# Kernel optimization log

Hardware: AMD Instinct MI355X
Metric: run time of the kernel (lower is better)

Reference implementation:

```python
import jax, jax.numpy as jnp
import numpy as np

DIM = 1024
HEADS = 16
HEAD_DIM = DIM // HEADS
SCALE = HEAD_DIM ** -0.5


def setup_inputs() -> dict:
    key = jax.random.key(0)
    ks = jax.random.split(key, 6)
    B, N, C = 2, 2048, DIM
    q = jax.random.normal(ks[0], (B, N, C), dtype=jnp.float32)
    k = jax.random.normal(ks[1], (B, N, C), dtype=jnp.float32)
    v = jax.random.normal(ks[2], (B, N, C), dtype=jnp.float32)
    # torch nn.Linear weights: out = x @ W.T (+ b); qkv has no bias (qkv_bias=False)
    W_qkv = jax.random.normal(ks[3], (3 * C, 3 * C), dtype=jnp.float32) * (3 * C) ** -0.5
    W_proj = jax.random.normal(ks[4], (C, C), dtype=jnp.float32) * C ** -0.5
    b_proj = jax.random.normal(ks[5], (C,), dtype=jnp.float32) * 0.02
    return {"q": q, "k": k, "v": v, "W_qkv": W_qkv, "W_proj": W_proj, "b_proj": b_proj}


def reference(q, k, v, W_qkv, W_proj, b_proj):
    B, N, C = q.shape
    # fused QKV projection on concatenated [q,k,v] -> [B,N,3C]
    qkv = jnp.concatenate([q, k, v], axis=-1) @ W_qkv.T
    qkv = qkv.reshape(B, N, 3, HEADS, HEAD_DIM).transpose(2, 0, 3, 1, 4)  # [3,B,H,N,hd]
    qh, kh, vh = qkv[0], qkv[1], qkv[2]
    attn = jnp.einsum('bhqd,bhkd->bhqk', qh, kh) * SCALE
    attn = jax.nn.softmax(attn, axis=-1)  # attn_drop is identity (p=0)
    x = jnp.einsum('bhqk,bhkd->bhqd', attn, vh)  # [B,H,N,hd]
    x = x.transpose(0, 2, 1, 3).reshape(B, N, C)
    x = x @ W_proj.T + b_proj  # proj_drop is identity (p=0)
    return x
```

## Files before the change

kernel.cpp:

```cpp
#include <hip/hip_runtime.h>
#include <hip/hip_bf16.h>
#include <stdint.h>

#define HEADS 16
#define HD 64
#define SEQ 2048
#define BATCH 2
#define CDIM 1024
#define MROWS (BATCH*SEQ)
#define K3C (3*CDIM)
#define QSCALE 0.1803368801111244f

typedef __bf16 bf16x8 __attribute__((ext_vector_type(8)));
typedef float  f32x4  __attribute__((ext_vector_type(4)));

__device__ __forceinline__ unsigned short f2bf(float f) {
    __hip_bfloat16 h = __float2bfloat16(f);
    return __builtin_bit_cast(unsigned short, h);
}
__device__ __forceinline__ unsigned int pack2bf(float a, float b) {
    return (unsigned int)f2bf(a) | ((unsigned int)f2bf(b) << 16);
}
__device__ __forceinline__ bf16x8 frag(uint4 u) { return __builtin_bit_cast(bf16x8, u); }

__device__ __forceinline__ void async16(const unsigned short* g, unsigned short* lds) {
    __builtin_amdgcn_global_load_lds(
        (const __attribute__((address_space(1))) unsigned int*)g,
        (__attribute__((address_space(3))) unsigned int*)lds, 16, 0, 0);
}

__device__ __forceinline__ void dsr(uint4& d, unsigned addr, unsigned imm) {
    asm volatile("ds_read_b128 %0, %1 offset:%c2" : "=v"(d) : "v"(addr), "i"(imm));
}

__global__ void cast_all(const float* __restrict__ q, const float* __restrict__ k,
                         const float* __restrict__ v, const float* __restrict__ Wq,
                         const float* __restrict__ Wp,
                         unsigned short* __restrict__ A, unsigned short* __restrict__ Wqb,
                         unsigned short* __restrict__ Wpb)
{
    const int bid = blockIdx.x;
    const int t = threadIdx.x;
    if (bid < MROWS) {
        const float* srcs[3] = {q, k, v};
        #pragma unroll
        for (int i = 0; i < 3; ++i) {
            float4 f = *(const float4*)(srcs[i] + (size_t)bid*CDIM + t*4);
            ushort4 s;
            s.x = f2bf(f.x); s.y = f2bf(f.y); s.z = f2bf(f.z); s.w = f2bf(f.w);
            *(ushort4*)(A + (size_t)bid*K3C + i*CDIM + t*4) = s;
        }
    } else if (bid < MROWS + 9216) {
        int idx = (bid - MROWS)*256 + t;
        float4 f = ((const float4*)Wq)[idx];
        ushort4 s;
        s.x = f2bf(f.x); s.y = f2bf(f.y); s.z = f2bf(f.z); s.w = f2bf(f.w);
        ((ushort4*)Wqb)[idx] = s;
    } else {
        int idx = (bid - MROWS - 9216)*256 + t;
        float4 f = ((const float4*)Wp)[idx];
        ushort4 s;
        s.x = f2bf(f.x); s.y = f2bf(f.y); s.z = f2bf(f.z); s.w = f2bf(f.w);
        ((ushort4*)Wpb)[idx] = s;
    }
}

template<int EPI>
__global__ __launch_bounds__(256, 2)
void gemm_bt(const unsigned short* __restrict__ A, const unsigned short* __restrict__ B,
             int M, int N, int K,
             unsigned short* __restrict__ qh, unsigned short* __restrict__ kh,
             unsigned short* __restrict__ vt,
             const float* __restrict__ bias, float* __restrict__ out)
{
    __shared__ __attribute__((aligned(16))) unsigned short As[128*32];
    __shared__ __attribute__((aligned(16))) unsigned short Bs[128*32];
    const int tid  = threadIdx.x;
    const int wave = tid >> 6;
    const int lane = tid & 63;
    const int l15  = lane & 15;
    const int quad = lane >> 4;
    const int wm = (wave >> 1) * 64;
    const int wn = (wave & 1) * 64;
    const int m0 = blockIdx.x * 128;
    const int n0 = blockIdx.y * 128;

    f32x4 acc[4][4] = {};

    const int srow = tid >> 2;
    const int sc8  = (tid & 3) * 8;

    for (int k0 = 0; k0 < K; k0 += 32) {
        #pragma unroll
        for (int t = 0; t < 2; ++t) {
            int row = t*64 + srow;
            const unsigned short* ga = A + (size_t)(m0 + row)*K + k0 + sc8;
            const unsigned short* gb = B + (size_t)(n0 + row)*K + k0 + sc8;
            async16(ga, &As[(t*256 + wave*64)*8]);
            async16(gb, &Bs[(t*256 + wave*64)*8]);
        }
        __syncthreads();
        uint4 af[4], bfv[4];
        #pragma unroll
        for (int i = 0; i < 4; ++i) {
            af[i]  = *(const uint4*)&As[(wm + i*16 + l15)*32 + quad*8];
            bfv[i] = *(const uint4*)&Bs[(wn + i*16 + l15)*32 + quad*8];
        }
        #pragma unroll
        for (int mi = 0; mi < 4; ++mi)
            #pragma unroll
            for (int ni = 0; ni < 4; ++ni)
                acc[mi][ni] = __builtin_amdgcn_mfma_f32_16x16x32_bf16(
                    frag(af[mi]), frag(bfv[ni]), acc[mi][ni], 0, 0, 0);
        __syncthreads();
    }

    if constexpr (EPI == 0) {
        #pragma unroll
        for (int mi = 0; mi < 4; ++mi) {
            int row0 = m0 + wm + mi*16 + quad*4;
            int b  = row0 >> 11;
            int nq = row0 & 2047;
            #pragma unroll
            for (int ni = 0; ni < 4; ++ni) {
                int col   = n0 + wn + ni*16 + l15;
                int which = col >> 10;
                int h     = (col >> 6) & 15;
                int d     = col & 63;
                int bh    = b*HEADS + h;
                if (which == 2) {
                    ushort4 pv;
                    pv.x = f2bf(acc[mi][ni][0]);
                    pv.y = f2bf(acc[mi][ni][1]);
                    pv.z = f2bf(acc[mi][ni][2]);
                    pv.w = f2bf(acc[mi][ni][3]);
                    *(ushort4*)&vt[((size_t)bh*HD + d)*SEQ + nq] = pv;
                } else {
                    unsigned short* dst = (which == 0) ? qh : kh;
                    float sc = (which == 0) ? QSCALE : 1.0f;
                    #pragma unroll
                    for (int r = 0; r < 4; ++r)
                        dst[((size_t)bh*SEQ + nq + r)*HD + d] = f2bf(acc[mi][ni][r] * sc);
                }
            }
        }
    } else {
        #pragma unroll
        for (int mi = 0; mi < 4; ++mi) {
            int row0 = m0 + wm + mi*16 + quad*4;
            #pragma unroll
            for (int ni = 0; ni < 4; ++ni) {
                int col  = n0 + wn + ni*16 + l15;
                float bv = bias[col];
                #pragma unroll
                for (int r = 0; r < 4; ++r)
                    out[(size_t)(row0 + r)*N + col] = acc[mi][ni][r] + bv;
            }
        }
    }
}

#define NT48 48

__global__ __launch_bounds__(512, 2)
void gemm256_qkv(const unsigned short* __restrict__ A, const unsigned short* __restrict__ B,
                 unsigned short* __restrict__ qh, unsigned short* __restrict__ kh,
                 unsigned short* __restrict__ vt)
{
    __shared__ __attribute__((aligned(16))) unsigned short As[2*16384];
    __shared__ __attribute__((aligned(16))) unsigned short Bs[2*12288];

    const int tid  = threadIdx.x;
    const int wave = tid >> 6;
    const int lane = tid & 63;
    const int l15  = lane & 15;
    const int quad = lane >> 4;
    const int wr   = wave >> 2;
    const int wc   = wave & 3;

    const int id  = blockIdx.x;
    const int swz = (id & 7)*32 + (id >> 3);
    const int m0  = (swz & 15) * 256;
    const int n0  = (swz >> 4) * 192;

    size_t aSrc[4]; size_t bSrc[3];
    #pragma unroll
    for (int u = 0; u < 4; ++u) {
        int P  = u*8192 + tid*16;
        int st = P >> 10, q = P & 1023;
        int ql = q ^ (((q >> 9) & 1) << 5);
        int row = m0 + (st >> 1)*16 + (ql >> 6);
        int kel = (st & 1)*32 + ((ql & 63) >> 1);
        aSrc[u] = (size_t)row*K3C + kel;
    }
    #pragma unroll
    for (int u = 0; u < 3; ++u) {
        int P  = u*8192 + tid*16;
        int st = P >> 10, q = P & 1023;
        int ql = q ^ (((q >> 9) & 1) << 5);
        int row = n0 + (st >> 1)*16 + (ql >> 6);
        int kel = (st & 1)*32 + ((ql & 63) >> 1);
        bSrc[u] = (size_t)row*K3C + kel;
    }
    const int wdst = wave*512;

    auto stage = [&](int t) {
        const int hb = t & 1;
        #pragma unroll
        for (int u = 0; u < 4; ++u)
            async16(A + aSrc[u] + t*64, As + hb*16384 + u*4096 + wdst);
        #pragma unroll
        for (int u = 0; u < 3; ++u)
            async16(B + bSrc[u] + t*64, Bs + hb*12288 + u*4096 + wdst);
    };

    const unsigned lanebyte = (unsigned)((l15*64 + quad*16) ^ ((l15 & 8) << 2));
    const unsigned aAddr = (unsigned)(uintptr_t)&As[0] + lanebyte + (unsigned)(wr*16384);
    const unsigned bAddr = (unsigned)(uintptr_t)&Bs[0] + lanebyte + (unsigned)(wc*6144);

    f32x4 acc[8][3] = {};

    stage(0); stage(1);
    asm volatile("s_waitcnt vmcnt(7)" ::: "memory");
    __builtin_amdgcn_s_barrier();

    for (int tt = 0; tt < NT48; tt += 2) {
        #pragma unroll
        for (int hb = 0; hb < 2; ++hb) {
            const int t = tt + hb;
            uint4 a0[8], b0[3], a1[8], b1[3];

            #pragma unroll
            for (int mi = 0; mi < 8; ++mi)
                dsr(a0[mi], aAddr, hb*32768 + mi*2048);
            #pragma unroll
            for (int ni = 0; ni < 3; ++ni)
                dsr(b0[ni], bAddr, hb*24576 + ni*2048);
            #pragma unroll
            for (int mi = 0; mi < 8; ++mi)
                dsr(a1[mi], aAddr, hb*32768 + mi*2048 + 1024);
            #pragma unroll
            for (int ni = 0; ni < 3; ++ni)
                dsr(b1[ni], bAddr, hb*24576 + ni*2048 + 1024);

            asm volatile("s_waitcnt lgkmcnt(11)" ::: "memory");
            __builtin_amdgcn_sched_barrier(0);
            __builtin_amdgcn_s_setprio(1);
            #pragma unroll
            for (int mi = 0; mi < 8; ++mi)
                #pragma unroll
                for (int ni = 0; ni < 3; ++ni)
                    acc[mi][ni] = __builtin_amdgcn_mfma_f32_16x16x32_bf16(
                        frag(a0[mi]), frag(b0[ni]), acc[mi][ni], 0, 0, 0);
            __builtin_amdgcn_s_setprio(0);

            asm volatile("s_waitcnt lgkmcnt(0)" ::: "memory");
            __builtin_amdgcn_sched_barrier(0);
            __builtin_amdgcn_s_barrier();

            __builtin_amdgcn_s_setprio(1);
            #pragma unroll
            for (int mi = 0; mi < 8; ++mi)
                #pragma unroll
                for (int ni = 0; ni < 3; ++ni)
                    acc[mi][ni] = __builtin_amdgcn_mfma_f32_16x16x32_bf16(
                        frag(a1[mi]), frag(b1[ni]), acc[mi][ni], 0, 0, 0);
            __builtin_amdgcn_s_setprio(0);

            if (t + 2 < NT48)      { stage(t + 2);
                                     asm volatile("s_waitcnt vmcnt(7)" ::: "memory"); }
            else if (t + 1 < NT48) { asm volatile("s_waitcnt vmcnt(0)" ::: "memory"); }
            __builtin_amdgcn_s_barrier();
        }
    }

    #pragma unroll
    for (int mi = 0; mi < 8; ++mi) {
        const int row0 = m0 + wr*128 + mi*16 + quad*4;
        const int b  = row0 >> 11;
        const int nq = row0 & 2047;
        #pragma unroll
        for (int ni = 0; ni < 3; ++ni) {
            const int col   = n0 + wc*48 + ni*16 + l15;
            const int which = col >> 10;
            const int h     = (col >> 6) & 15;
            const int d     = col & 63;
            const int bh_   = b*HEADS + h;
            if (which == 2) {
                ushort4 pv;
                pv.x = f2bf(acc[mi][ni][0]);
                pv.y = f2bf(acc[mi][ni][1]);
                pv.z = f2bf(acc[mi][ni][2]);
                pv.w = f2bf(acc[mi][ni][3]);
                *(ushort4*)&vt[((size_t)bh_*HD + d)*SEQ + nq] = pv;
            } else {
                unsigned short* dst = (which == 0) ? qh : kh;
                float sc = (which == 0) ? QSCALE : 1.0f;
                #pragma unroll
                for (int r = 0; r < 4; ++r)
                    dst[((size_t)bh_*SEQ + nq + r)*HD + d] = f2bf(acc[mi][ni][r] * sc);
            }
        }
    }
}

__global__ __launch_bounds__(256, 2)
void attention(const unsigned short* __restrict__ qh, const unsigned short* __restrict__ kh,
               const unsigned short* __restrict__ vt, unsigned short* __restrict__ xb)
{
    const int qt = blockIdx.x;
    const int h  = blockIdx.y;
    const int b  = blockIdx.z;
    const int bh = b*HEADS + h;
    const int tid  = threadIdx.x;
    const int wave = tid >> 6;
    const int lane = tid & 63;
    const int l15  = lane & 15;
    const int quad = lane >> 4;

    __shared__ __attribute__((aligned(16))) unsigned short Ks[2][64*64];
    __shared__ __attribute__((aligned(16))) unsigned short Vs[2][64*64];
    __shared__ __attribute__((aligned(16))) unsigned short Ps[4][2*16*72];

    const unsigned short* Qp = qh + ((size_t)bh*SEQ + qt*128 + wave*32)*HD;
    const unsigned short* Kp = kh + (size_t)bh*SEQ*HD;
    const unsigned short* Vp = vt + (size_t)bh*HD*SEQ;

    auto stage = [&](int kt, int bufI) {
        #pragma unroll
        for (int t = 0; t < 2; ++t) {
            int c  = t*256 + wave*64 + lane;
            int r  = c >> 3;
            int cc = (c & 7) ^ (r & 7);
            async16(Kp + (size_t)(kt*64 + r)*HD + cc*8,
                    &Ks[bufI][(t*256 + wave*64)*8]);
            async16(Vp + (size_t)r*SEQ + kt*64 + cc*8,
                    &Vs[bufI][(t*256 + wave*64)*8]);
        }
    };

    stage(0, 0);

    uint4 qf[2][2];
    #pragma unroll
    for (int g = 0; g < 2; ++g) {
        qf[g][0] = *(const uint4*)(Qp + (size_t)(g*16 + l15)*HD + quad*8);
        qf[g][1] = *(const uint4*)(Qp + (size_t)(g*16 + l15)*HD + 32 + quad*8);
    }

    f32x4 o[2][4] = {};
    float m_s[2] = {-INFINITY, -INFINITY};
    float l_s[2] = {0.f, 0.f};

    unsigned short* Pw = Ps[wave];
    const int x7 = l15 & 7;

    for (int kt = 0; kt < SEQ/64; ++kt) {
        stage((kt + 1) & 31, (kt + 1) & 1);
        asm volatile("s_waitcnt vmcnt(4)" ::: "memory");
        asm volatile("s_barrier" ::: "memory");

        const unsigned short* Kb = Ks[kt & 1];
        const unsigned short* Vb = Vs[kt & 1];

        f32x4 s[2][4];
        #pragma unroll
        for (int st = 0; st < 4; ++st) {
            int rb = st*16 + l15;
            uint4 kf0 = *(const uint4*)&Kb[(rb*8 + (quad ^ x7))*8];
            uint4 kf1 = *(const uint4*)&Kb[(rb*8 + ((4 + quad) ^ x7))*8];
            #pragma unroll
            for (int g = 0; g < 2; ++g) {
                f32x4 z = {};
                z = __builtin_amdgcn_mfma_f32_16x16x32_bf16(frag(kf0), frag(qf[g][0]), z, 0, 0, 0);
                z = __builtin_amdgcn_mfma_f32_16x16x32_bf16(frag(kf1), frag(qf[g][1]), z, 0, 0, 0);
                s[g][st] = z;
            }
        }

        #pragma unroll
        for (int g = 0; g < 2; ++g) {
            float mloc = s[g][0][0];
            #pragma unroll
            for (int st = 0; st < 4; ++st)
                #pragma unroll
                for (int r = 0; r < 4; ++r)
                    mloc = fmaxf(mloc, s[g][st][r]);
            mloc = fmaxf(mloc, __shfl_xor(mloc, 16));
            mloc = fmaxf(mloc, __shfl_xor(mloc, 32));

            float mn = fmaxf(m_s[g], mloc);
            float al = __builtin_amdgcn_exp2f(m_s[g] - mn);
            m_s[g] = mn;

            float rs = 0.f;
            float p[4][4];
            #pragma unroll
            for (int st = 0; st < 4; ++st)
                #pragma unroll
                for (int r = 0; r < 4; ++r) {
                    p[st][r] = __builtin_amdgcn_exp2f(s[g][st][r] - mn);
                    rs += p[st][r];
                }
            rs += __shfl_xor(rs, 16);
            rs += __shfl_xor(rs, 32);
            l_s[g] = al*l_s[g] + rs;

            #pragma unroll
            for (int st = 0; st < 4; ++st)
                #pragma unroll
                for (int r = 0; r < 4; ++r)
                    o[g][st][r] *= al;

            #pragma unroll
            for (int st = 0; st < 4; ++st) {
                uint2 pk;
                pk.x = pack2bf(p[st][0], p[st][1]);
                pk.y = pack2bf(p[st][2], p[st][3]);
                *(uint2*)&Pw[g*1152 + l15*72 + st*16 + quad*4] = pk;
            }
        }
        asm volatile("s_waitcnt lgkmcnt(0)" ::: "memory");

        uint4 pB[2][2];
        #pragma unroll
        for (int g = 0; g < 2; ++g) {
            pB[g][0] = *(const uint4*)&Pw[g*1152 + l15*72 + quad*8];
            pB[g][1] = *(const uint4*)&Pw[g*1152 + l15*72 + 32 + quad*8];
        }

        #pragma unroll
        for (int st = 0; st < 4; ++st) {
            int rb = st*16 + l15;
            uint4 vf0 = *(const uint4*)&Vb[(rb*8 + (quad ^ x7))*8];
            uint4 vf1 = *(const uint4*)&Vb[(rb*8 + ((4 + quad) ^ x7))*8];
            #pragma unroll
            for (int g = 0; g < 2; ++g) {
                o[g][st] = __builtin_amdgcn_mfma_f32_16x16x32_bf16(frag(vf0), frag(pB[g][0]), o[g][st], 0, 0, 0);
                o[g][st] = __builtin_amdgcn_mfma_f32_16x16x32_bf16(frag(vf1), frag(pB[g][1]), o[g][st], 0, 0, 0);
            }
        }

        asm volatile("s_barrier" ::: "memory");
    }

    #pragma unroll
    for (int g = 0; g < 2; ++g) {
        float inv = 1.0f / l_s[g];
        #pragma unroll
        for (int st = 0; st < 4; ++st) {
            uint2 pk;
            pk.x = pack2bf(o[g][st][0]*inv, o[g][st][1]*inv);
            pk.y = pack2bf(o[g][st][2]*inv, o[g][st][3]*inv);
            *(uint2*)&Pw[g*1152 + l15*72 + st*16 + quad*4] = pk;
        }
    }
    asm volatile("s_waitcnt lgkmcnt(0)" ::: "memory");

    const int qr = lane >> 2;
    const int dd = (lane & 3) * 16;
    #pragma unroll
    for (int g = 0; g < 2; ++g) {
        uint4 oa = *(const uint4*)&Pw[g*1152 + qr*72 + dd];
        uint4 ob = *(const uint4*)&Pw[g*1152 + qr*72 + dd + 8];
        const int mrow = b*SEQ + qt*128 + wave*32 + g*16 + qr;
        *(uint4*)&xb[(size_t)mrow*CDIM + h*HD + dd]     = oa;
        *(uint4*)&xb[(size_t)mrow*CDIM + h*HD + dd + 8] = ob;
    }
}

extern "C" void kernel_launch(void* const* d_in, const int* in_sizes, int n_in,
                              void* d_out, int out_size, void* d_ws, size_t ws_size,
                              hipStream_t stream)
{
    const float* q  = (const float*)d_in[0];
    const float* k  = (const float*)d_in[1];
    const float* v  = (const float*)d_in[2];
    const float* Wq = (const float*)d_in[3];
    const float* Wp = (const float*)d_in[4];
    const float* bp = (const float*)d_in[5];
    float* out = (float*)d_out;

    char* p = (char*)d_ws;
    auto carve = [&](size_t bytes) { char* r = p; p += (bytes + 255) & ~(size_t)255; return r; };
    unsigned short* Abuf   = (unsigned short*)carve((size_t)MROWS*K3C*2);
    unsigned short* Wqkvb  = (unsigned short*)carve((size_t)K3C*K3C*2);
    unsigned short* Wprojb = (unsigned short*)carve((size_t)CDIM*CDIM*2);
    unsigned short* qhb    = (unsigned short*)carve((size_t)BATCH*HEADS*SEQ*HD*2);
    unsigned short* khb    = (unsigned short*)carve((size_t)BATCH*HEADS*SEQ*HD*2);
    unsigned short* vtb    = (unsigned short*)carve((size_t)BATCH*HEADS*SEQ*HD*2);
    unsigned short* xbuf   = (unsigned short*)carve((size_t)MROWS*CDIM*2);

    cast_all<<<MROWS + 9216 + 1024, 256, 0, stream>>>(q, k, v, Wq, Wp, Abuf, Wqkvb, Wprojb);

    gemm256_qkv<<<dim3(256), 512, 0, stream>>>(Abuf, Wqkvb, qhb, khb, vtb);

    attention<<<dim3(SEQ/128, HEADS, BATCH), 256, 0, stream>>>(qhb, khb, vtb, xbuf);

    gemm_bt<1><<<dim3(MROWS/128, CDIM/128), 256, 0, stream>>>(
        xbuf, Wprojb, MROWS, CDIM, CDIM, nullptr, nullptr, nullptr, bp, out);
}
```

Measured before the change: 284.8 us.

## Permute V layout to feed P from registers and skip redundant softmax rescales

The QKV projection now writes V^T with its key index permuted within each 64-block. The bf16 P values produced by the S MFMA can then be used directly as B operands of the PV MFMA, with no LDS round trip through a per-wave buffer. K and V fragments are loaded up front through explicit ds_read address arithmetic, with waitcnt and sched_barrier controlling issue order. Online-softmax rescaling of O and l is skipped unless the running max grows by more than 8 (log2 domain), which saves VALU multiplies but lets exp2 values reach up to 2^8 before rescaling and relies on the permuted layout being exactly right.

```diff
diff --git a/kernel.cpp b/kernel.cpp
--- a/kernel.cpp
+++ b/kernel.cpp
@@ -292,7 +292,9 @@
                 pv.y = f2bf(acc[mi][ni][1]);
                 pv.z = f2bf(acc[mi][ni][2]);
                 pv.w = f2bf(acc[mi][ni][3]);
-                *(ushort4*)&vt[((size_t)bh_*HD + d)*SEQ + nq] = pv;
+                const int st_ = mi & 3;
+                const int nq2 = (nq & ~63) | ((quad + ((st_ >> 1) << 2)) << 3) | ((st_ & 1) << 2);
+                *(ushort4*)&vt[((size_t)bh_*HD + d)*SEQ + nq2] = pv;
             } else {
                 unsigned short* dst = (which == 0) ? qh : kh;
                 float sc = (which == 0) ? QSCALE : 1.0f;
@@ -352,32 +354,42 @@
     float m_s[2] = {-INFINITY, -INFINITY};
     float l_s[2] = {0.f, 0.f};
 
-    unsigned short* Pw = Ps[wave];
     const int x7 = l15 & 7;
+    const unsigned ksBase = (unsigned)(uintptr_t)&Ks[0][0];
+    const unsigned vsBase = (unsigned)(uintptr_t)&Vs[0][0];
+    const unsigned laneA  = (unsigned)(l15*128 + (quad ^ x7)*16);
+    const unsigned laneB  = (unsigned)(l15*128 + ((quad ^ x7) ^ 4)*16);
 
     for (int kt = 0; kt < SEQ/64; ++kt) {
         stage((kt + 1) & 31, (kt + 1) & 1);
         asm volatile("s_waitcnt vmcnt(4)" ::: "memory");
         asm volatile("s_barrier" ::: "memory");
 
-        const unsigned short* Kb = Ks[kt & 1];
-        const unsigned short* Vb = Vs[kt & 1];
+        const unsigned bufo = (unsigned)((kt & 1) * 8192);
+        const unsigned ka = ksBase + bufo + laneA, kb = ksBase + bufo + laneB;
+        const unsigned va = vsBase + bufo + laneA, vb = vsBase + bufo + laneB;
+
+        uint4 kf[4][2], vf[4][2];
+        #pragma unroll
+        for (int st = 0; st < 4; ++st) { dsr(kf[st][0], ka, st*2048); dsr(kf[st][1], kb, st*2048); }
+        #pragma unroll
+        for (int st = 0; st < 4; ++st) { dsr(vf[st][0], va, st*2048); dsr(vf[st][1], vb, st*2048); }
+
+        asm volatile("s_waitcnt lgkmcnt(8)" ::: "memory");
+        __builtin_amdgcn_sched_barrier(0);
 
         f32x4 s[2][4];
         #pragma unroll
-        for (int st = 0; st < 4; ++st) {
-            int rb = st*16 + l15;
-            uint4 kf0 = *(const uint4*)&Kb[(rb*8 + (quad ^ x7))*8];
-            uint4 kf1 = *(const uint4*)&Kb[(rb*8 + ((4 + quad) ^ x7))*8];
+        for (int st = 0; st < 4; ++st)
             #pragma unroll
             for (int g = 0; g < 2; ++g) {
                 f32x4 z = {};
-                z = __builtin_amdgcn_mfma_f32_16x16x32_bf16(frag(kf0), frag(qf[g][0]), z, 0, 0, 0);
-                z = __builtin_amdgcn_mfma_f32_16x16x32_bf16(frag(kf1), frag(qf[g][1]), z, 0, 0, 0);
+                z = __builtin_amdgcn_mfma_f32_16x16x32_bf16(frag(kf[st][0]), frag(qf[g][0]), z, 0, 0, 0);
+                z = __builtin_amdgcn_mfma_f32_16x16x32_bf16(frag(kf[st][1]), frag(qf[g][1]), z, 0, 0, 0);
                 s[g][st] = z;
             }
-        }
-
+
+        unsigned W[2][8];
         #pragma unroll
         for (int g = 0; g < 2; ++g) {
             float mloc = s[g][0][0];
@@ -389,9 +401,18 @@
             mloc = fmaxf(mloc, __shfl_xor(mloc, 16));
             mloc = fmaxf(mloc, __shfl_xor(mloc, 32));
 
-            float mn = fmaxf(m_s[g], mloc);
-            float al = __builtin_amdgcn_exp2f(m_s[g] - mn);
-            m_s[g] = mn;
+            if (!__all(mloc - m_s[g] <= 8.0f)) {
+                float mn = fmaxf(m_s[g], mloc);
+                float al = __builtin_amdgcn_exp2f(m_s[g] - mn);
+                m_s[g] = mn;
+                l_s[g] *= al;
+                #pragma unroll
+                for (int st = 0; st < 4; ++st)
+                    #pragma unroll
+                    for (int r = 0; r < 4; ++r)
+                        o[g][st][r] *= al;
+            }
+            const float mn = m_s[g];
 
             float rs = 0.f;
             float p[4][4];
@@ -404,46 +425,34 @@
                 }
             rs += __shfl_xor(rs, 16);
             rs += __shfl_xor(rs, 32);
-            l_s[g] = al*l_s[g] + rs;
-
-            #pragma unroll
-            for (int st = 0; st < 4; ++st)
-                #pragma unroll
-                for (int r = 0; r < 4; ++r)
-                    o[g][st][r] *= al;
+            l_s[g] += rs;
 
             #pragma unroll
             for (int st = 0; st < 4; ++st) {
-                uint2 pk;
-                pk.x = pack2bf(p[st][0], p[st][1]);
-                pk.y = pack2bf(p[st][2], p[st][3]);
-                *(uint2*)&Pw[g*1152 + l15*72 + st*16 + quad*4] = pk;
-            }
-        }
+                W[g][st*2 + 0] = pack2bf(p[st][0], p[st][1]);
+                W[g][st*2 + 1] = pack2bf(p[st][2], p[st][3]);
+            }
+        }
+
         asm volatile("s_waitcnt lgkmcnt(0)" ::: "memory");
-
-        uint4 pB[2][2];
+        __builtin_amdgcn_sched_barrier(0);
+
         #pragma unroll
         for (int g = 0; g < 2; ++g) {
-            pB[g][0] = *(const uint4*)&Pw[g*1152 + l15*72 + quad*8];
-            pB[g][1] = *(const uint4*)&Pw[g*1152 + l15*72 + 32 + quad*8];
-        }
-
-        #pragma unroll
-        for (int st = 0; st < 4; ++st) {
-            int rb = st*16 + l15;
-            uint4 vf0 = *(const uint4*)&Vb[(rb*8 + (quad ^ x7))*8];
-            uint4 vf1 = *(const uint4*)&Vb[(rb*8 + ((4 + quad) ^ x7))*8];
-            #pragma unroll
-            for (int g = 0; g < 2; ++g) {
-                o[g][st] = __builtin_amdgcn_mfma_f32_16x16x32_bf16(frag(vf0), frag(pB[g][0]), o[g][st], 0, 0, 0);
-                o[g][st] = __builtin_amdgcn_mfma_f32_16x16x32_bf16(frag(vf1), frag(pB[g][1]), o[g][st], 0, 0, 0);
+            uint4 pb0, pb1;
+            pb0.x = W[g][0]; pb0.y = W[g][1]; pb0.z = W[g][2]; pb0.w = W[g][3];
+            pb1.x = W[g][4]; pb1.y = W[g][5]; pb1.z = W[g][6]; pb1.w = W[g][7];
+            #pragma unroll
+            for (int st = 0; st < 4; ++st) {
+                o[g][st] = __builtin_amdgcn_mfma_f32_16x16x32_bf16(frag(vf[st][0]), frag(pb0), o[g][st], 0, 0, 0);
+                o[g][st] = __builtin_amdgcn_mfma_f32_16x16x32_bf16(frag(vf[st][1]), frag(pb1), o[g][st], 0, 0, 0);
             }
         }
 
         asm volatile("s_barrier" ::: "memory");
     }
 
+    unsigned short* Pw = Ps[wave];
     #pragma unroll
     for (int g = 0; g < 2; ++g) {
         float inv = 1.0f / l_s[g];
@@ -456,6 +465,7 @@
         }
     }
     asm volatile("s_waitcnt lgkmcnt(0)" ::: "memory");
+    __syncthreads();
 
     const int qr = lane >> 2;
     const int dd = (lane & 3) * 16;
```

New measurement: 272.3 us. 1.05x faster.
